# Performance work log

Measured on AMD Instinct MI355X. Metric: run time of the kernel, lower is better.

Reference implementation:

```python
import jax, jax.numpy as jnp
import numpy as np

E = 512   # embed_dim
H = 16    # num_heads
D = E // H  # head_dim = 32
L = 2048  # target (query) length
S = 2048  # source (stored pattern) length
N = 4     # batch
LN_EPS = 1e-5


def setup_inputs() -> dict:
    key = jax.random.key(0)
    ks = jax.random.split(key, 8)
    inv_sqrt_e = 1.0 / np.sqrt(E).astype(np.float32)
    return {
        "query": jax.random.normal(ks[0], (L, N, E), jnp.float32),
        "key_in": jax.random.normal(ks[1], (S, N, E), jnp.float32),
        "value": jax.random.normal(ks[2], (S, N, E), jnp.float32),
        "scaling": jax.random.uniform(ks[3], (H,), jnp.float32),  # per-head beta
        "in_proj_weight": jax.random.normal(ks[4], (3 * E, E), jnp.float32) * inv_sqrt_e,
        "in_proj_bias": jnp.zeros((3 * E,), jnp.float32),
        "p_norm_weight": jnp.ones((D,), jnp.float32),
        "p_norm_bias": jnp.zeros((D,), jnp.float32),
        "out_proj_weight": jax.random.normal(ks[5], (E, E), jnp.float32) * inv_sqrt_e,
        "out_proj_bias": jnp.zeros((E,), jnp.float32),
    }


def reference(query, key_in, value, scaling, in_proj_weight, in_proj_bias,
              p_norm_weight, p_norm_bias, out_proj_weight, out_proj_bias):
    Lq, Nb, Ed = query.shape
    Sk = key_in.shape[0]
    # split packed in-projection (torch Linear convention: y = x @ W^T + b)
    wq, wk, wv = jnp.split(in_proj_weight, 3, axis=0)
    bq, bk, bv = jnp.split(in_proj_bias, 3, axis=0)
    q = jnp.einsum('lne,fe->lnf', query, wq) + bq
    k = jnp.einsum('sne,fe->snf', key_in, wk) + bk
    v = jnp.einsum('sne,fe->snf', value, wv) + bv
    # (len, N, H*D) -> (N, H, len, D)
    q = q.reshape(Lq, Nb, H, D).transpose(1, 2, 0, 3)
    k = k.reshape(Sk, Nb, H, D).transpose(1, 2, 0, 3)
    v = v.reshape(Sk, Nb, H, D).transpose(1, 2, 0, 3)

    def pattern_norm(x):
        # affine LayerNorm over the association (head) dimension D
        mu = jnp.mean(x, axis=-1, keepdims=True)
        var = jnp.mean(jnp.square(x - mu), axis=-1, keepdims=True)
        return (x - mu) * jax.lax.rsqrt(var + LN_EPS) * p_norm_weight + p_norm_bias

    k = pattern_norm(k)
    v = pattern_norm(v)

    beta = scaling.reshape(1, H, 1, 1)  # per-head inverse-temperature
    scores = jnp.einsum('nhld,nhsd->nhls', q * beta, k)  # [N,H,L,S]
    attn = jax.nn.softmax(scores, axis=-1)  # single Hopfield update (update_steps_max=0)
    out = jnp.einsum('nhls,nhsd->nhld', attn, v)  # [N,H,L,D]
    out = out.transpose(2, 0, 1, 3).reshape(Lq, Nb, H * D)
    out = jnp.einsum('lnf,of->lno', out, out_proj_weight) + out_proj_bias
    return out  # (L, N, E)
```

## Files before the change

kernel.cpp:

```cpp
#include <hip/hip_runtime.h>
#include <cstdint>

#define LN_EPS 1e-5f

typedef _Float16 f16;
typedef _Float16 half4_t __attribute__((ext_vector_type(4)));
typedef _Float16 half8_t __attribute__((ext_vector_type(8)));
typedef __fp16 fp16v2 __attribute__((ext_vector_type(2)));
typedef float f32x4 __attribute__((ext_vector_type(4)));

__device__ __forceinline__ void gl_lds16(const void* g, void* l) {
    __builtin_amdgcn_global_load_lds(
        (__attribute__((address_space(1))) void*)(uintptr_t)g,
        (__attribute__((address_space(3))) void*)(uint32_t)(uintptr_t)l,
        16, 0, 0);
}

__device__ __forceinline__ half4_t pack4(float a, float b, float c, float d) {
    fp16v2 lo = __builtin_amdgcn_cvt_pkrtz(a, b);
    fp16v2 hi = __builtin_amdgcn_cvt_pkrtz(c, d);
    half4_t r;
    r[0] = (f16)lo[0]; r[1] = (f16)lo[1]; r[2] = (f16)hi[0]; r[3] = (f16)hi[1];
    return r;
}

__global__ void k_cast(const float* __restrict__ W1f, const float* __restrict__ W2f,
                       const float* __restrict__ Xq, const float* __restrict__ Xk,
                       const float* __restrict__ Xv,
                       f16* __restrict__ W1h, f16* __restrict__ W2h,
                       f16* __restrict__ Xh) {
    int t = blockIdx.x * blockDim.x + threadIdx.x;
    const float4* src;
    half4_t* dst;
    int idx;
    if (t < 196608)      { src = (const float4*)W1f; dst = (half4_t*)W1h; idx = t; }
    else if (t < 262144) { src = (const float4*)W2f; dst = (half4_t*)W2h; idx = t - 196608; }
    else {
        int u = t - 262144;
        int s = u >> 20;
        idx = u & 1048575;
        src = (s == 0) ? (const float4*)Xq : ((s == 1) ? (const float4*)Xk : (const float4*)Xv);
        dst = (half4_t*)(Xh + (size_t)s * 4194304);
    }
    float4 v = src[idx];
    dst[idx] = pack4(v.x, v.y, v.z, v.w);
}

__global__ __launch_bounds__(256) void k_inproj(
    const f16* __restrict__ Xh, const f16* __restrict__ W1,
    const float* __restrict__ bias, const float* __restrict__ scaling,
    f16* __restrict__ Qg, f16* __restrict__ Kg, f16* __restrict__ Vg)
{
    __shared__ __align__(16) f16 Al[128 * 32];
    __shared__ __align__(16) f16 Bl[128 * 32];

    const int tid = threadIdx.x;
    const int m0 = blockIdx.x * 128;
    const int f0 = blockIdx.y * 128;
    const int sec = f0 >> 9;
    const f16* X = Xh + (size_t)sec * 4194304;
    f16* Ob = (sec == 0) ? Qg : ((sec == 1) ? Kg : Vg);

    const int wid = tid >> 6, ln = tid & 63, l15 = ln & 15, quad = ln >> 4;
    const int wm = wid >> 1, wn = wid & 1;

    f32x4 z4 = {0.f, 0.f, 0.f, 0.f};
    f32x4 acc[4][4];
    #pragma unroll
    for (int i = 0; i < 4; ++i)
        #pragma unroll
        for (int j = 0; j < 4; ++j) acc[i][j] = z4;

    for (int kt = 0; kt < 16; ++kt) {
        const int k0 = kt * 32;
        #pragma unroll
        for (int i = 0; i < 2; ++i) {
            int row = wid * 32 + i * 16 + (ln >> 2);
            int co = (ln & 3) * 8;
            gl_lds16(W1 + (size_t)(f0 + row) * 512 + k0 + co,
                     Bl + (wid * 32 + i * 16) * 32);
            gl_lds16(X + (size_t)(m0 + row) * 512 + k0 + co,
                     Al + (wid * 32 + i * 16) * 32);
        }
        __syncthreads();

        half8_t a[4], b[4];
        #pragma unroll
        for (int i = 0; i < 4; ++i)
            a[i] = *(const half8_t*)(Al + (wm * 64 + i * 16 + l15) * 32 + quad * 8);
        #pragma unroll
        for (int j = 0; j < 4; ++j)
            b[j] = *(const half8_t*)(Bl + (wn * 64 + j * 16 + l15) * 32 + quad * 8);
        #pragma unroll
        for (int i = 0; i < 4; ++i)
            #pragma unroll
            for (int j = 0; j < 4; ++j)
                acc[i][j] = __builtin_amdgcn_mfma_f32_16x16x32_f16(b[j], a[i], acc[i][j], 0, 0, 0);
        __syncthreads();
    }

    #pragma unroll
    for (int j = 0; j < 4; ++j) {
        int fb = f0 + wn * 64 + j * 16;
        int floc = (fb & 511) + quad * 4;
        int hh = floc >> 5;
        int cc = (floc >> 3) & 3, e0 = floc & 7;
        float sc2 = (sec == 0) ? scaling[hh] * 1.44269504f : 1.0f;
        float4 bs4 = *(const float4*)(bias + fb + quad * 4);
        #pragma unroll
        for (int i = 0; i < 4; ++i) {
            int rm = m0 + wm * 64 + i * 16 + l15;
            int l = rm >> 2, nb = rm & 3;
            int gg = nb * 16 + hh;
            *(half4_t*)(Ob + (size_t)gg * 65536 + (size_t)cc * 16384 + (size_t)l * 8 + e0) =
                pack4((acc[i][j][0] + bs4.x) * sc2, (acc[i][j][1] + bs4.y) * sc2,
                      (acc[i][j][2] + bs4.z) * sc2, (acc[i][j][3] + bs4.w) * sc2);
        }
    }
}

__global__ void k_norm_kv(f16* __restrict__ Kg, const f16* __restrict__ Vg,
                          const float* __restrict__ w, const float* __restrict__ b,
                          f16* __restrict__ Vtg) {
    __shared__ __align__(16) f16 T[32 * 64];
    const int t = threadIdx.x;
    const int seg = blockIdx.x, g = blockIdx.y;
    const int s_l = t >> 2, c = t & 3;
    const size_t base = (size_t)g * 65536 + (size_t)c * 16384 + (size_t)(seg * 64 + s_l) * 8;

    half8_t kv = *(const half8_t*)(Kg + base);
    half8_t vv = *(const half8_t*)(Vg + base);
    float kf[8], vf[8];
    float ks1 = 0.f, ks2 = 0.f, vs1 = 0.f, vs2 = 0.f;
    #pragma unroll
    for (int j = 0; j < 8; ++j) {
        kf[j] = (float)kv[j]; ks1 += kf[j]; ks2 += kf[j] * kf[j];
        vf[j] = (float)vv[j]; vs1 += vf[j]; vs2 += vf[j] * vf[j];
    }
    ks1 += __shfl_xor(ks1, 1); ks1 += __shfl_xor(ks1, 2);
    ks2 += __shfl_xor(ks2, 1); ks2 += __shfl_xor(ks2, 2);
    vs1 += __shfl_xor(vs1, 1); vs1 += __shfl_xor(vs1, 2);
    vs2 += __shfl_xor(vs2, 1); vs2 += __shfl_xor(vs2, 2);
    float kmu = ks1 * (1.f / 32.f), kvar = ks2 * (1.f / 32.f) - kmu * kmu;
    float vmu = vs1 * (1.f / 32.f), vvar = vs2 * (1.f / 32.f) - vmu * vmu;
    float krs = rsqrtf(kvar + LN_EPS), vrs = rsqrtf(vvar + LN_EPS);

    half8_t ky;
    int cs = s_l >> 3, es = s_l & 7;
    #pragma unroll
    for (int j = 0; j < 8; ++j) {
        int d = c * 8 + j;
        float wd = w[d], bd = b[d];
        ky[j] = (f16)((kf[j] - kmu) * krs * wd + bd);
        T[d * 64 + (cs ^ j) * 8 + es] = (f16)((vf[j] - vmu) * vrs * wd + bd);
    }
    *(half8_t*)(Kg + base) = ky;
    __syncthreads();
    int d_o = t >> 3, c_o = t & 7;
    half8_t out = *(const half8_t*)(T + d_o * 64 + c_o * 8);
    *(half8_t*)(Vtg + (size_t)(g * 32 + seg) * 2048 + d_o * 64 + c_o * 8) = out;
}

__global__ __launch_bounds__(256, 4) void k_flash(
    const f16* __restrict__ Qg, const f16* __restrict__ Kg,
    const f16* __restrict__ Vtg, f16* __restrict__ Og)
{
    __shared__ __align__(16) char smem[32768];

    const int tid = threadIdx.x, wid = tid >> 6, ln = tid & 63;
    const int l15 = ln & 15, quad = ln >> 4, l8 = ln & 7;
    char* Pw = smem + 16384 + wid * 4096;
    const int g = blockIdx.x, h = g & 15, n = g >> 4;
    const int q0 = blockIdx.y * 128;

    const f16* Qb = Qg + (size_t)g * 65536 + (size_t)wid * 16384 + (size_t)q0 * 8;
    gl_lds16(Qb + (size_t)ln * 8,        smem + 16384 + wid * 2048);
    gl_lds16(Qb + (size_t)(64 + ln) * 8, smem + 16384 + wid * 2048 + 1024);
    const f16* kp = Kg + (size_t)g * 65536 + (size_t)wid * 16384;
    const f16* vp = Vtg + (size_t)(g * 32) * 2048 + wid * 512;
    gl_lds16(kp + (size_t)ln * 8, smem + wid * 1024);
    gl_lds16(vp + (size_t)ln * 8, smem + 8192 + wid * 1024);
    kp += 512;
    vp += 2048;
    __builtin_amdgcn_s_waitcnt(0x0F70);
    __syncthreads();
    half8_t aq[2];
    #pragma unroll
    for (int i = 0; i < 2; ++i)
        aq[i] = *(const half8_t*)(smem + 16384 + quad * 2048 + (wid * 32 + i * 16 + l15) * 16);
    __syncthreads();

    half8_t onesf;
    {
        f16 o = (l15 == 0) ? (f16)1.0f : (f16)0.0f;
        #pragma unroll
        for (int j = 0; j < 8; ++j) onesf[j] = o;
    }

    f32x4 z4 = {0.f, 0.f, 0.f, 0.f};
    f32x4 accO[2][2], accSum[2];
    accO[0][0] = z4; accO[0][1] = z4; accO[1][0] = z4; accO[1][1] = z4;
    accSum[0] = z4; accSum[1] = z4;
    float m_i[2] = {-1e30f, -1e30f};

    for (int st = 0; st < 32; ++st) {
        const int cur = st & 1;
        if (st < 31) {
            gl_lds16(kp + (size_t)ln * 8, smem + (cur ^ 1) * 4096 + wid * 1024);
            gl_lds16(vp + (size_t)ln * 8, smem + 8192 + (cur ^ 1) * 4096 + wid * 1024);
            kp += 512;
            vp += 2048;
        }
        const char* Kl = smem + cur * 4096;
        const char* Vt = smem + 8192 + cur * 4096;

        half8_t ak[4];
        #pragma unroll
        for (int mt = 0; mt < 4; ++mt)
            ak[mt] = *(const half8_t*)(Kl + quad * 1024 + (mt * 16 + l15) * 16);
        f32x4 accS[2][4];
        #pragma unroll
        for (int i = 0; i < 2; ++i)
            #pragma unroll
            for (int mt = 0; mt < 4; ++mt)
                accS[i][mt] = __builtin_amdgcn_mfma_f32_16x16x32_f16(ak[mt], aq[i], z4, 0, 0, 0);

        float mn[2];
        bool up = false;
        #pragma unroll
        for (int i = 0; i < 2; ++i) {
            float xm = fmaxf(fmaxf(accS[i][0][0], accS[i][0][1]),
                             fmaxf(accS[i][0][2], accS[i][0][3]));
            #pragma unroll
            for (int mt = 1; mt < 4; ++mt)
                xm = fmaxf(xm, fmaxf(fmaxf(accS[i][mt][0], accS[i][mt][1]),
                                     fmaxf(accS[i][mt][2], accS[i][mt][3])));
            xm = fmaxf(xm, __shfl_xor(xm, 16));
            xm = fmaxf(xm, __shfl_xor(xm, 32));
            up = up || (xm > m_i[i]);
            mn[i] = fmaxf(m_i[i], xm);
        }
        if (__ballot(up)) {
            #pragma unroll
            for (int i = 0; i < 2; ++i) {
                float alpha = __builtin_amdgcn_exp2f(m_i[i] - mn[i]);
                #pragma unroll
                for (int dt = 0; dt < 2; ++dt)
                    #pragma unroll
                    for (int r = 0; r < 4; ++r) accO[i][dt][r] *= alpha;
                #pragma unroll
                for (int r = 0; r < 4; ++r) accSum[i][r] *= alpha;
            }
        }
        m_i[0] = mn[0]; m_i[1] = mn[1];

        #pragma unroll
        for (int i = 0; i < 2; ++i) {
            #pragma unroll
            for (int mt = 0; mt < 4; ++mt) {
                float p0 = __builtin_amdgcn_exp2f(accS[i][mt][0] - mn[i]);
                float p1 = __builtin_amdgcn_exp2f(accS[i][mt][1] - mn[i]);
                float p2 = __builtin_amdgcn_exp2f(accS[i][mt][2] - mn[i]);
                float p3 = __builtin_amdgcn_exp2f(accS[i][mt][3] - mn[i]);
                int ch = (mt * 2 + (quad >> 1)) ^ l8;
                *(half4_t*)(Pw + (i * 16 + l15) * 128 + ch * 16 + (quad & 1) * 8) =
                    pack4(p0, p1, p2, p3);
            }
        }

        #pragma unroll
        for (int kt = 0; kt < 2; ++kt) {
            half8_t av[2], bp[2];
            #pragma unroll
            for (int dt = 0; dt < 2; ++dt) {
                int d = dt * 16 + l15;
                int cp = (kt * 4 + quad) ^ (l15 & 7);
                av[dt] = *(const half8_t*)(Vt + d * 128 + cp * 16);
            }
            #pragma unroll
            for (int i = 0; i < 2; ++i)
                bp[i] = *(const half8_t*)(Pw + (i * 16 + l15) * 128 +
                                          (((kt * 4 + quad) ^ l8) * 16));
            #pragma unroll
            for (int i = 0; i < 2; ++i) {
                #pragma unroll
                for (int dt = 0; dt < 2; ++dt)
                    accO[i][dt] = __builtin_amdgcn_mfma_f32_16x16x32_f16(av[dt], bp[i], accO[i][dt], 0, 0, 0);
                accSum[i] = __builtin_amdgcn_mfma_f32_16x16x32_f16(onesf, bp[i], accSum[i], 0, 0, 0);
            }
        }

        __builtin_amdgcn_s_waitcnt(0x0F70);
        __syncthreads();
    }

    #pragma unroll
    for (int i = 0; i < 2; ++i) {
        float li = __shfl(accSum[i][0], l15);
        float inv = 1.f / li;
        #pragma unroll
        for (int dt = 0; dt < 2; ++dt)
            *(half4_t*)(Pw + (i * 16 + l15) * 80 + (dt * 16 + quad * 4) * 2) =
                pack4(accO[i][dt][0] * inv, accO[i][dt][1] * inv,
                      accO[i][dt][2] * inv, accO[i][dt][3] * inv);
    }
    int q2 = ln >> 1, hf = ln & 1;
    half8_t o0 = *(const half8_t*)(Pw + q2 * 80 + hf * 32);
    half8_t o1 = *(const half8_t*)(Pw + q2 * 80 + hf * 32 + 16);
    size_t rowe = ((size_t)(n * 2048 + q0 + wid * 32 + q2)) * 512 + h * 32 + hf * 16;
    *(half8_t*)(Og + rowe) = o0;
    *(half8_t*)(Og + rowe + 8) = o1;
}

__global__ __launch_bounds__(256) void k_outproj(
    const f16* __restrict__ A, const f16* __restrict__ W2,
    const float* __restrict__ bias, float* __restrict__ Out)
{
    __shared__ __align__(16) f16 Al[128 * 32];
    __shared__ __align__(16) f16 Bl[128 * 32];

    const int tid = threadIdx.x;
    const int m0 = blockIdx.x * 128;
    const int f0 = blockIdx.y * 128;
    const int wid = tid >> 6, ln = tid & 63, l15 = ln & 15, quad = ln >> 4;
    const int wm = wid >> 1, wn = wid & 1;

    f32x4 z4 = {0.f, 0.f, 0.f, 0.f};
    f32x4 acc[4][4];
    #pragma unroll
    for (int i = 0; i < 4; ++i)
        #pragma unroll
        for (int j = 0; j < 4; ++j) acc[i][j] = z4;

    for (int kt = 0; kt < 16; ++kt) {
        const int k0 = kt * 32;
        #pragma unroll
        for (int i = 0; i < 2; ++i) {
            int row = wid * 32 + i * 16 + (ln >> 2);
            gl_lds16(A + (size_t)(m0 + row) * 512 + k0 + (ln & 3) * 8,
                     Al + (wid * 32 + i * 16) * 32);
            gl_lds16(W2 + (size_t)(f0 + row) * 512 + k0 + (ln & 3) * 8,
                     Bl + (wid * 32 + i * 16) * 32);
        }
        __syncthreads();

        half8_t a[4], b[4];
        #pragma unroll
        for (int i = 0; i < 4; ++i)
            a[i] = *(const half8_t*)(Al + (wm * 64 + i * 16 + l15) * 32 + quad * 8);
        #pragma unroll
        for (int j = 0; j < 4; ++j)
            b[j] = *(const half8_t*)(Bl + (wn * 64 + j * 16 + l15) * 32 + quad * 8);
        #pragma unroll
        for (int i = 0; i < 4; ++i)
            #pragma unroll
            for (int j = 0; j < 4; ++j)
                acc[i][j] = __builtin_amdgcn_mfma_f32_16x16x32_f16(b[j], a[i], acc[i][j], 0, 0, 0);
        __syncthreads();
    }

    #pragma unroll
    for (int j = 0; j < 4; ++j) {
        int fb = f0 + wn * 64 + j * 16;
        float4 bs4 = *(const float4*)(bias + fb + quad * 4);
        #pragma unroll
        for (int i = 0; i < 4; ++i) {
            int rm = m0 + wm * 64 + i * 16 + l15;
            int orow = (rm & 2047) * 4 + (rm >> 11);
            float4 o;
            o.x = acc[i][j][0] + bs4.x;
            o.y = acc[i][j][1] + bs4.y;
            o.z = acc[i][j][2] + bs4.z;
            o.w = acc[i][j][3] + bs4.w;
            *(float4*)(Out + (size_t)orow * 512 + fb + quad * 4) = o;
        }
    }
}

extern "C" void kernel_launch(void* const* d_in, const int* in_sizes, int n_in,
                              void* d_out, int out_size, void* d_ws, size_t ws_size,
                              hipStream_t stream) {
    const float* query   = (const float*)d_in[0];
    const float* key_in  = (const float*)d_in[1];
    const float* value   = (const float*)d_in[2];
    const float* scaling = (const float*)d_in[3];
    const float* ipw     = (const float*)d_in[4];
    const float* ipb     = (const float*)d_in[5];
    const float* pnw     = (const float*)d_in[6];
    const float* pnb     = (const float*)d_in[7];
    const float* opw     = (const float*)d_in[8];
    const float* opb     = (const float*)d_in[9];
    float* out = (float*)d_out;

    f16* Qg  = (f16*)d_ws;
    f16* Kg  = Qg + (size_t)4194304;
    f16* Vg  = Qg + (size_t)8388608;
    f16* W1  = Qg + (size_t)12582912;
    f16* W2  = Qg + (size_t)13369344;
    f16* Xh  = Qg + (size_t)13631488;
    f16* Vtg = Xh;
    f16* Og  = Vg;

    k_cast<<<13312, 256, 0, stream>>>(ipw, opw, query, key_in, value, W1, W2, Xh);
    k_inproj<<<dim3(64, 12), 256, 0, stream>>>(Xh, W1, ipb, scaling, Qg, Kg, Vg);
    k_norm_kv<<<dim3(32, 64), 256, 0, stream>>>(Kg, Vg, pnw, pnb, Vtg);
    k_flash<<<dim3(64, 16), 256, 0, stream>>>(Qg, Kg, Vtg, Og);
    k_outproj<<<dim3(64, 4), 256, 0, stream>>>(Og, W2, opb, out);
}
```

Baseline: 225.7 us.

## Halve flash query tile per block, raise occupancy, add lazy softmax rescale

The flash-attention kernel now handles 64 queries per block (16 per wave) instead of 128, doubling the grid. Q is loaded straight from global into registers instead of staged through LDS, and the LDS footprint and register state shrink, allowing a launch bound of 6 blocks per CU. The online-softmax rescale now fires only when the new row max exceeds the running max by more than 8 (log2 domain). This avoids most rescales, at the cost of exp2 values up to 2^8 that could lose fp16 headroom. Each K/V tile is now reused by half as many queries, so total K/V traffic from global memory doubles.

Result: no change. 228.5 us (+1.2%).

```diff
diff --git a/kernel.cpp b/kernel.cpp
--- a/kernel.cpp
+++ b/kernel.cpp
@@ -161,21 +161,21 @@
     *(half8_t*)(Vtg + (size_t)(g * 32 + seg) * 2048 + d_o * 64 + c_o * 8) = out;
 }
 
-__global__ __launch_bounds__(256, 4) void k_flash(
+__global__ __launch_bounds__(256, 6) void k_flash(
     const f16* __restrict__ Qg, const f16* __restrict__ Kg,
     const f16* __restrict__ Vtg, f16* __restrict__ Og)
 {
-    __shared__ __align__(16) char smem[32768];
+    __shared__ __align__(16) char smem[24576];
 
     const int tid = threadIdx.x, wid = tid >> 6, ln = tid & 63;
     const int l15 = ln & 15, quad = ln >> 4, l8 = ln & 7;
-    char* Pw = smem + 16384 + wid * 4096;
+    char* Pw = smem + 16384 + wid * 2048;
     const int g = blockIdx.x, h = g & 15, n = g >> 4;
-    const int q0 = blockIdx.y * 128;
-
-    const f16* Qb = Qg + (size_t)g * 65536 + (size_t)wid * 16384 + (size_t)q0 * 8;
-    gl_lds16(Qb + (size_t)ln * 8,        smem + 16384 + wid * 2048);
-    gl_lds16(Qb + (size_t)(64 + ln) * 8, smem + 16384 + wid * 2048 + 1024);
+    const int q0 = blockIdx.y * 64;
+
+    half8_t aq = *(const half8_t*)(Qg + (size_t)g * 65536 + (size_t)quad * 16384 +
+                                   (size_t)(q0 + wid * 16 + l15) * 8);
+
     const f16* kp = Kg + (size_t)g * 65536 + (size_t)wid * 16384;
     const f16* vp = Vtg + (size_t)(g * 32) * 2048 + wid * 512;
     gl_lds16(kp + (size_t)ln * 8, smem + wid * 1024);
@@ -184,11 +184,6 @@
     vp += 2048;
     __builtin_amdgcn_s_waitcnt(0x0F70);
     __syncthreads();
-    half8_t aq[2];
-    #pragma unroll
-    for (int i = 0; i < 2; ++i)
-        aq[i] = *(const half8_t*)(smem + 16384 + quad * 2048 + (wid * 32 + i * 16 + l15) * 16);
-    __syncthreads();
 
     half8_t onesf;
     {
@@ -198,10 +193,9 @@
     }
 
     f32x4 z4 = {0.f, 0.f, 0.f, 0.f};
-    f32x4 accO[2][2], accSum[2];
-    accO[0][0] = z4; accO[0][1] = z4; accO[1][0] = z4; accO[1][1] = z4;
-    accSum[0] = z4; accSum[1] = z4;
-    float m_i[2] = {-1e30f, -1e30f};
+    f32x4 accO[2], accSum;
+    accO[0] = z4; accO[1] = z4; accSum = z4;
+    float m_i = -1e30f;
 
     for (int st = 0; st < 32; ++st) {
         const int cur = st & 1;
@@ -218,98 +212,72 @@
         #pragma unroll
         for (int mt = 0; mt < 4; ++mt)
             ak[mt] = *(const half8_t*)(Kl + quad * 1024 + (mt * 16 + l15) * 16);
-        f32x4 accS[2][4];
-        #pragma unroll
-        for (int i = 0; i < 2; ++i)
-            #pragma unroll
-            for (int mt = 0; mt < 4; ++mt)
-                accS[i][mt] = __builtin_amdgcn_mfma_f32_16x16x32_f16(ak[mt], aq[i], z4, 0, 0, 0);
-
-        float mn[2];
-        bool up = false;
-        #pragma unroll
-        for (int i = 0; i < 2; ++i) {
-            float xm = fmaxf(fmaxf(accS[i][0][0], accS[i][0][1]),
-                             fmaxf(accS[i][0][2], accS[i][0][3]));
-            #pragma unroll
-            for (int mt = 1; mt < 4; ++mt)
-                xm = fmaxf(xm, fmaxf(fmaxf(accS[i][mt][0], accS[i][mt][1]),
-                                     fmaxf(accS[i][mt][2], accS[i][mt][3])));
-            xm = fmaxf(xm, __shfl_xor(xm, 16));
-            xm = fmaxf(xm, __shfl_xor(xm, 32));
-            up = up || (xm > m_i[i]);
-            mn[i] = fmaxf(m_i[i], xm);
-        }
-        if (__ballot(up)) {
-            #pragma unroll
-            for (int i = 0; i < 2; ++i) {
-                float alpha = __builtin_amdgcn_exp2f(m_i[i] - mn[i]);
+        f32x4 accS[4];
+        #pragma unroll
+        for (int mt = 0; mt < 4; ++mt)
+            accS[mt] = __builtin_amdgcn_mfma_f32_16x16x32_f16(ak[mt], aq, z4, 0, 0, 0);
+
+        float xm = fmaxf(fmaxf(accS[0][0], accS[0][1]), fmaxf(accS[0][2], accS[0][3]));
+        #pragma unroll
+        for (int mt = 1; mt < 4; ++mt)
+            xm = fmaxf(xm, fmaxf(fmaxf(accS[mt][0], accS[mt][1]),
+                                 fmaxf(accS[mt][2], accS[mt][3])));
+        xm = fmaxf(xm, __shfl_xor(xm, 16));
+        xm = fmaxf(xm, __shfl_xor(xm, 32));
+        if (__ballot(xm > m_i + 8.f)) {
+            float mn = fmaxf(m_i, xm);
+            float alpha = __builtin_amdgcn_exp2f(m_i - mn);
+            #pragma unroll
+            for (int dt = 0; dt < 2; ++dt)
                 #pragma unroll
-                for (int dt = 0; dt < 2; ++dt)
-                    #pragma unroll
-                    for (int r = 0; r < 4; ++r) accO[i][dt][r] *= alpha;
-                #pragma unroll
-                for (int r = 0; r < 4; ++r) accSum[i][r] *= alpha;
-            }
-        }
-        m_i[0] = mn[0]; m_i[1] = mn[1];
-
-        #pragma unroll
-        for (int i = 0; i < 2; ++i) {
-            #pragma unroll
-            for (int mt = 0; mt < 4; ++mt) {
-                float p0 = __builtin_amdgcn_exp2f(accS[i][mt][0] - mn[i]);
-                float p1 = __builtin_amdgcn_exp2f(accS[i][mt][1] - mn[i]);
-                float p2 = __builtin_amdgcn_exp2f(accS[i][mt][2] - mn[i]);
-                float p3 = __builtin_amdgcn_exp2f(accS[i][mt][3] - mn[i]);
-                int ch = (mt * 2 + (quad >> 1)) ^ l8;
-                *(half4_t*)(Pw + (i * 16 + l15) * 128 + ch * 16 + (quad & 1) * 8) =
-                    pack4(p0, p1, p2, p3);
-            }
+                for (int r = 0; r < 4; ++r) accO[dt][r] *= alpha;
+            #pragma unroll
+            for (int r = 0; r < 4; ++r) accSum[r] *= alpha;
+            m_i = mn;
+        }
+
+        #pragma unroll
+        for (int mt = 0; mt < 4; ++mt) {
+            float p0 = __builtin_amdgcn_exp2f(accS[mt][0] - m_i);
+            float p1 = __builtin_amdgcn_exp2f(accS[mt][1] - m_i);
+            float p2 = __builtin_amdgcn_exp2f(accS[mt][2] - m_i);
+            float p3 = __builtin_amdgcn_exp2f(accS[mt][3] - m_i);
+            int ch = (mt * 2 + (quad >> 1)) ^ l8;
+            *(half4_t*)(Pw + l15 * 128 + ch * 16 + (quad & 1) * 8) =
+                pack4(p0, p1, p2, p3);
         }
 
         #pragma unroll
         for (int kt = 0; kt < 2; ++kt) {
-            half8_t av[2], bp[2];
+            half8_t av[2], bp;
             #pragma unroll
             for (int dt = 0; dt < 2; ++dt) {
                 int d = dt * 16 + l15;
                 int cp = (kt * 4 + quad) ^ (l15 & 7);
                 av[dt] = *(const half8_t*)(Vt + d * 128 + cp * 16);
             }
-            #pragma unroll
-            for (int i = 0; i < 2; ++i)
-                bp[i] = *(const half8_t*)(Pw + (i * 16 + l15) * 128 +
-                                          (((kt * 4 + quad) ^ l8) * 16));
-            #pragma unroll
-            for (int i = 0; i < 2; ++i) {
-                #pragma unroll
-                for (int dt = 0; dt < 2; ++dt)
-                    accO[i][dt] = __builtin_amdgcn_mfma_f32_16x16x32_f16(av[dt], bp[i], accO[i][dt], 0, 0, 0);
-                accSum[i] = __builtin_amdgcn_mfma_f32_16x16x32_f16(onesf, bp[i], accSum[i], 0, 0, 0);
-            }
+            bp = *(const half8_t*)(Pw + l15 * 128 + (((kt * 4 + quad) ^ l8) * 16));
+            #pragma unroll
+            for (int dt = 0; dt < 2; ++dt)
+                accO[dt] = __builtin_amdgcn_mfma_f32_16x16x32_f16(av[dt], bp, accO[dt], 0, 0, 0);
+            accSum = __builtin_amdgcn_mfma_f32_16x16x32_f16(onesf, bp, accSum, 0, 0, 0);
         }
 
         __builtin_amdgcn_s_waitcnt(0x0F70);
         __syncthreads();
     }
 
-    #pragma unroll
-    for (int i = 0; i < 2; ++i) {
-        float li = __shfl(accSum[i][0], l15);
-        float inv = 1.f / li;
-        #pragma unroll
-        for (int dt = 0; dt < 2; ++dt)
-            *(half4_t*)(Pw + (i * 16 + l15) * 80 + (dt * 16 + quad * 4) * 2) =
-                pack4(accO[i][dt][0] * inv, accO[i][dt][1] * inv,
-                      accO[i][dt][2] * inv, accO[i][dt][3] * inv);
-    }
-    int q2 = ln >> 1, hf = ln & 1;
-    half8_t o0 = *(const half8_t*)(Pw + q2 * 80 + hf * 32);
-    half8_t o1 = *(const half8_t*)(Pw + q2 * 80 + hf * 32 + 16);
-    size_t rowe = ((size_t)(n * 2048 + q0 + wid * 32 + q2)) * 512 + h * 32 + hf * 16;
+    float li = __shfl(accSum[0], l15);
+    float inv = 1.f / li;
+    #pragma unroll
+    for (int dt = 0; dt < 2; ++dt)
+        *(half4_t*)(Pw + l15 * 80 + (dt * 16 + quad * 4) * 2) =
+            pack4(accO[dt][0] * inv, accO[dt][1] * inv,
+                  accO[dt][2] * inv, accO[dt][3] * inv);
+    int q2 = ln >> 2, c4 = ln & 3;
+    half8_t o0 = *(const half8_t*)(Pw + q2 * 80 + c4 * 16);
+    size_t rowe = ((size_t)(n * 2048 + q0 + wid * 16 + q2)) * 512 + h * 32 + c4 * 8;
     *(half8_t*)(Og + rowe) = o0;
-    *(half8_t*)(Og + rowe + 8) = o1;
 }
 
 __global__ __launch_bounds__(256) void k_outproj(
@@ -404,6 +372,6 @@
     k_cast<<<13312, 256, 0, stream>>>(ipw, opw, query, key_in, value, W1, W2, Xh);
     k_inproj<<<dim3(64, 12), 256, 0, stream>>>(Xh, W1, ipb, scaling, Qg, Kg, Vg);
     k_norm_kv<<<dim3(32, 64), 256, 0, stream>>>(Kg, Vg, pnw, pnb, Vtg);
-    k_flash<<<dim3(64, 16), 256, 0, stream>>>(Qg, Kg, Vtg, Og);
+    k_flash<<<dim3(64, 32), 256, 0, stream>>>(Qg, Kg, Vtg, Og);
     k_outproj<<<dim3(64, 4), 256, 0, stream>>>(Og, W2, opb, out);
 }
```

## Triple-buffer K/V tiles in flash kernel with one barrier per step

Applied to the files above, without the earlier changes.

Moves the K/V LDS staging from double to triple buffering with two tiles in flight. Each step now waits with vmcnt and a single barrier instead of a waitcnt plus syncthreads at the end. Q fragments are loaded straight from global into registers instead of going through LDS. It also adds s_setprio around the MFMA blocks and a lazy max update that rescales only when the max grows by more than 8. This raises LDS use per block and risks fp16 overflow headroom in P through the lazy-rescale threshold.

Measured after the change: 220.7 us. -2.2%, faster.

```diff
diff --git a/kernel.cpp b/kernel.cpp
--- a/kernel.cpp
+++ b/kernel.cpp
@@ -165,30 +165,28 @@
     const f16* __restrict__ Qg, const f16* __restrict__ Kg,
     const f16* __restrict__ Vtg, f16* __restrict__ Og)
 {
-    __shared__ __align__(16) char smem[32768];
+    __shared__ __align__(16) char smem[40960];
 
     const int tid = threadIdx.x, wid = tid >> 6, ln = tid & 63;
     const int l15 = ln & 15, quad = ln >> 4, l8 = ln & 7;
-    char* Pw = smem + 16384 + wid * 4096;
+    char* Pw = smem + 24576 + wid * 4096;
     const int g = blockIdx.x, h = g & 15, n = g >> 4;
     const int q0 = blockIdx.y * 128;
 
-    const f16* Qb = Qg + (size_t)g * 65536 + (size_t)wid * 16384 + (size_t)q0 * 8;
-    gl_lds16(Qb + (size_t)ln * 8,        smem + 16384 + wid * 2048);
-    gl_lds16(Qb + (size_t)(64 + ln) * 8, smem + 16384 + wid * 2048 + 1024);
+    half8_t aq[2];
+    #pragma unroll
+    for (int i = 0; i < 2; ++i)
+        aq[i] = *(const half8_t*)(Qg + (size_t)g * 65536 + (size_t)quad * 16384 +
+                                  (size_t)(q0 + wid * 32 + i * 16 + l15) * 8);
+
     const f16* kp = Kg + (size_t)g * 65536 + (size_t)wid * 16384;
     const f16* vp = Vtg + (size_t)(g * 32) * 2048 + wid * 512;
     gl_lds16(kp + (size_t)ln * 8, smem + wid * 1024);
-    gl_lds16(vp + (size_t)ln * 8, smem + 8192 + wid * 1024);
-    kp += 512;
-    vp += 2048;
-    __builtin_amdgcn_s_waitcnt(0x0F70);
-    __syncthreads();
-    half8_t aq[2];
-    #pragma unroll
-    for (int i = 0; i < 2; ++i)
-        aq[i] = *(const half8_t*)(smem + 16384 + quad * 2048 + (wid * 32 + i * 16 + l15) * 16);
-    __syncthreads();
+    gl_lds16(vp + (size_t)ln * 8, smem + 12288 + wid * 1024);
+    gl_lds16(kp + 512 + (size_t)ln * 8, smem + 4096 + wid * 1024);
+    gl_lds16(vp + 2048 + (size_t)ln * 8, smem + 12288 + 4096 + wid * 1024);
+    kp += 1024;
+    vp += 4096;
 
     half8_t onesf;
     {
@@ -203,27 +201,34 @@
     accSum[0] = z4; accSum[1] = z4;
     float m_i[2] = {-1e30f, -1e30f};
 
+    int cur = 0;
     for (int st = 0; st < 32; ++st) {
-        const int cur = st & 1;
-        if (st < 31) {
-            gl_lds16(kp + (size_t)ln * 8, smem + (cur ^ 1) * 4096 + wid * 1024);
-            gl_lds16(vp + (size_t)ln * 8, smem + 8192 + (cur ^ 1) * 4096 + wid * 1024);
+        if (st < 31) asm volatile("s_waitcnt vmcnt(2)" ::: "memory");
+        else         asm volatile("s_waitcnt vmcnt(0)" ::: "memory");
+        __builtin_amdgcn_s_barrier();
+
+        if (st < 30) {
+            int nb = cur + 2; if (nb >= 3) nb -= 3;
+            gl_lds16(kp + (size_t)ln * 8, smem + nb * 4096 + wid * 1024);
+            gl_lds16(vp + (size_t)ln * 8, smem + 12288 + nb * 4096 + wid * 1024);
             kp += 512;
             vp += 2048;
         }
         const char* Kl = smem + cur * 4096;
-        const char* Vt = smem + 8192 + cur * 4096;
+        const char* Vt = smem + 12288 + cur * 4096;
 
         half8_t ak[4];
         #pragma unroll
         for (int mt = 0; mt < 4; ++mt)
             ak[mt] = *(const half8_t*)(Kl + quad * 1024 + (mt * 16 + l15) * 16);
         f32x4 accS[2][4];
+        __builtin_amdgcn_s_setprio(1);
         #pragma unroll
         for (int i = 0; i < 2; ++i)
             #pragma unroll
             for (int mt = 0; mt < 4; ++mt)
                 accS[i][mt] = __builtin_amdgcn_mfma_f32_16x16x32_f16(ak[mt], aq[i], z4, 0, 0, 0);
+        __builtin_amdgcn_s_setprio(0);
 
         float mn[2];
         bool up = false;
@@ -237,7 +242,7 @@
                                      fmaxf(accS[i][mt][2], accS[i][mt][3])));
             xm = fmaxf(xm, __shfl_xor(xm, 16));
             xm = fmaxf(xm, __shfl_xor(xm, 32));
-            up = up || (xm > m_i[i]);
+            up = up || (xm > m_i[i] + 8.f);
             mn[i] = fmaxf(m_i[i], xm);
         }
         if (__ballot(up)) {
@@ -250,18 +255,18 @@
                     for (int r = 0; r < 4; ++r) accO[i][dt][r] *= alpha;
                 #pragma unroll
                 for (int r = 0; r < 4; ++r) accSum[i][r] *= alpha;
+                m_i[i] = mn[i];
             }
         }
-        m_i[0] = mn[0]; m_i[1] = mn[1];
 
         #pragma unroll
         for (int i = 0; i < 2; ++i) {
             #pragma unroll
             for (int mt = 0; mt < 4; ++mt) {
-                float p0 = __builtin_amdgcn_exp2f(accS[i][mt][0] - mn[i]);
-                float p1 = __builtin_amdgcn_exp2f(accS[i][mt][1] - mn[i]);
-                float p2 = __builtin_amdgcn_exp2f(accS[i][mt][2] - mn[i]);
-                float p3 = __builtin_amdgcn_exp2f(accS[i][mt][3] - mn[i]);
+                float p0 = __builtin_amdgcn_exp2f(accS[i][mt][0] - m_i[i]);
+                float p1 = __builtin_amdgcn_exp2f(accS[i][mt][1] - m_i[i]);
+                float p2 = __builtin_amdgcn_exp2f(accS[i][mt][2] - m_i[i]);
+                float p3 = __builtin_amdgcn_exp2f(accS[i][mt][3] - m_i[i]);
                 int ch = (mt * 2 + (quad >> 1)) ^ l8;
                 *(half4_t*)(Pw + (i * 16 + l15) * 128 + ch * 16 + (quad & 1) * 8) =
                     pack4(p0, p1, p2, p3);
@@ -281,6 +286,7 @@
             for (int i = 0; i < 2; ++i)
                 bp[i] = *(const half8_t*)(Pw + (i * 16 + l15) * 128 +
                                           (((kt * 4 + quad) ^ l8) * 16));
+            __builtin_amdgcn_s_setprio(1);
             #pragma unroll
             for (int i = 0; i < 2; ++i) {
                 #pragma unroll
@@ -288,10 +294,10 @@
                     accO[i][dt] = __builtin_amdgcn_mfma_f32_16x16x32_f16(av[dt], bp[i], accO[i][dt], 0, 0, 0);
                 accSum[i] = __builtin_amdgcn_mfma_f32_16x16x32_f16(onesf, bp[i], accSum[i], 0, 0, 0);
             }
-        }
-
-        __builtin_amdgcn_s_waitcnt(0x0F70);
-        __syncthreads();
+            __builtin_amdgcn_s_setprio(0);
+        }
+
+        cur = cur + 1; if (cur == 3) cur = 0;
     }
 
     #pragma unroll
```
